# Optimization experiments

Measured on AMD Instinct MI355X. Metric: run time of the kernel, lower is better.

Reference implementation:

```python
import jax, jax.numpy as jnp
import numpy as np

N_HEAD = 16
D_QK = 128
D_V = 128
D_MODEL = 2048
BATCH = 2
SEQ = 2048


def alibi_slopes(n_head):
    # standard ALiBi slopes: 2^(-8*i/n_head) for i = 1..n_head
    return jnp.asarray(2.0 ** (-8.0 * np.arange(1, n_head + 1) / n_head), dtype=jnp.float32)


def setup_inputs() -> dict:
    key = jax.random.key(0)
    k1, k2, k3, k4, k5 = jax.random.split(key, 5)
    x = jax.random.normal(k1, (BATCH, SEQ, D_MODEL), dtype=jnp.float32)
    # causal attention mask (1 = keep, 0 = masked), broadcast over heads
    causal = jnp.tril(jnp.ones((SEQ, SEQ), dtype=bool))
    attention_mask = jnp.broadcast_to(causal, (BATCH, 1, SEQ, SEQ))
    Wq = jax.random.normal(k2, (D_MODEL, N_HEAD * D_QK), dtype=jnp.float32) * (D_MODEL ** -0.5)
    Wk = jax.random.normal(k3, (D_MODEL, N_HEAD * D_QK), dtype=jnp.float32) * (D_MODEL ** -0.5)
    Wv = jax.random.normal(k4, (D_MODEL, N_HEAD * D_V), dtype=jnp.float32) * (D_MODEL ** -0.5)
    Wo = jax.random.normal(k5, (N_HEAD * D_V, D_MODEL), dtype=jnp.float32) * ((N_HEAD * D_V) ** -0.5)
    return {"x": x, "attention_mask": attention_mask, "Wq": Wq, "Wk": Wk, "Wv": Wv, "Wo": Wo}


def reference(x, attention_mask, Wq, Wk, Wv, Wo):
    B, S, _ = x.shape
    scale = D_QK ** -0.5
    q = (x @ Wq).reshape(B, S, N_HEAD, D_QK).transpose(0, 2, 1, 3)  # [B,H,S,dqk]
    k = (x @ Wk).reshape(B, S, N_HEAD, D_QK).transpose(0, 2, 1, 3)
    v = (x @ Wv).reshape(B, S, N_HEAD, D_V).transpose(0, 2, 1, 3)
    scores = jnp.einsum('bhid,bhjd->bhij', q, k) * scale  # [B,H,S,S]
    # ALiBi bias: slope_h * (j - i), negative penalty for distant past keys
    pos = jnp.arange(S, dtype=jnp.float32)
    rel = pos[None, :] - pos[:, None]  # [S,S]
    slopes = alibi_slopes(N_HEAD)
    scores = scores + slopes[None, :, None, None] * rel[None, None, :, :]
    scores = jnp.where(attention_mask, scores, jnp.float32(-jnp.inf))
    attn = jax.nn.softmax(scores, axis=-1)
    out = jnp.einsum('bhij,bhjd->bhid', attn, v)  # [B,H,S,dv]
    out = out.transpose(0, 2, 1, 3).reshape(B, S, N_HEAD * D_V)
    return out @ Wo
```

## Files before the change

### kernel.cpp

```cpp
#include <hip/hip_runtime.h>
#include <cstdint>

typedef unsigned short u16;
typedef __attribute__((ext_vector_type(4))) u16 u16x4;
typedef __attribute__((ext_vector_type(8))) u16 u16x8;
typedef __attribute__((ext_vector_type(8))) __bf16 bf16x8;
typedef __attribute__((ext_vector_type(4))) float f32x4;

#define LOG2E 1.44269504088896340736f

static __device__ __forceinline__ u16 f2bf(float f) {
  unsigned u = __builtin_bit_cast(unsigned, f);
  u += 0x7fffu + ((u >> 16) & 1u);
  return (u16)(u >> 16);
}
static __device__ __forceinline__ float bf2f(u16 v) {
  unsigned u = ((unsigned)v) << 16;
  return __builtin_bit_cast(float, u);
}


static __device__ __forceinline__ void gload16(const u16* g, u16* l) {
  __builtin_amdgcn_global_load_lds(
      (__attribute__((address_space(1))) void*)(uintptr_t)g,
      (__attribute__((address_space(3))) void*)(uintptr_t)l, 16, 0, 0);
}

static __device__ __forceinline__ bf16x8 lds_bf8(const void* p) {
  return __builtin_bit_cast(bf16x8, *(const u16x8*)p);
}

__global__ __launch_bounds__(256) void cast_x_kernel(const float* __restrict__ src,
                                                     u16* __restrict__ dst) {
  int i = (blockIdx.x * 256 + threadIdx.x) * 4;
  float4 v = *(const float4*)(src + i);
  u16x4 r = {f2bf(v.x), f2bf(v.y), f2bf(v.z), f2bf(v.w)};
  *(u16x4*)(dst + i) = r;
}

__global__ __launch_bounds__(256) void transpose_w4_kernel(const float* Wq, const float* Wk,
                                                           const float* Wv, const float* Wo,
                                                           u16* Wqt, u16* Wkt, u16* Wvt,
                                                           u16* Wot) {
  const float* src = blockIdx.z == 0 ? Wq : (blockIdx.z == 1 ? Wk : (blockIdx.z == 2 ? Wv : Wo));
  u16* dst = blockIdx.z == 0 ? Wqt : (blockIdx.z == 1 ? Wkt : (blockIdx.z == 2 ? Wvt : Wot));
  __shared__ float tile[32][33];
  const int n0 = blockIdx.x * 32, k0 = blockIdx.y * 32;
  const int tx = threadIdx.x & 31, ty = threadIdx.x >> 5;
#pragma unroll
  for (int r = 0; r < 4; ++r) {
    int row = r * 8 + ty;
    tile[row][tx] = src[(size_t)(k0 + row) * 2048 + n0 + tx];
  }
  __syncthreads();
#pragma unroll
  for (int r = 0; r < 4; ++r) {
    int row = r * 8 + ty;
    dst[(size_t)(n0 + row) * 2048 + k0 + tx] = f2bf(tile[tx][row]);
  }
}

#define GSTAGE(TILE, KH, BUF)                                                        \
  do {                                                                               \
    const int bk = (TILE) * 64 + (KH) * 32;                                          \
    u16* as_ = &lds[((BUF) * 2 + (KH)) * 8192];                                      \
    u16* bs_ = &lds[32768 + ((BUF) * 2 + (KH)) * 8192];                              \
    gload16(&A[(size_t)(m0 + sr) * 2048 + bk + scu], as_ + tid * 8);                 \
    gload16(&A[(size_t)(m0 + 128 + sr) * 2048 + bk + scu], as_ + 4096 + tid * 8);    \
    gload16(&Bt[(size_t)(n0 + sr) * 2048 + bk + scu], bs_ + tid * 8);                \
    gload16(&Bt[(size_t)(n0 + 128 + sr) * 2048 + bk + scu], bs_ + 4096 + tid * 8);   \
  } while (0)

#define GPH(BUF, KH, STAGE_STMT, VMLIT)                                              \
  do {                                                                               \
    const u16* as_ = &lds[((BUF) * 2 + (KH)) * 8192];                                \
    const u16* bs_ = &lds[32768 + ((BUF) * 2 + (KH)) * 8192];                        \
    bf16x8 af[8], bq[4];                                                             \
    _Pragma("unroll") for (int mf = 0; mf < 8; ++mf) {                               \
      const int ar = wm * 128 + mf * 16 + l16;                                       \
      af[mf] = lds_bf8(&as_[(ar * 32 + lg * 8) ^ xsw]);                              \
    }                                                                                \
    _Pragma("unroll") for (int nf = 0; nf < 4; ++nf) {                               \
      const int br = wn * 64 + nf * 16 + l16;                                        \
      bq[nf] = lds_bf8(&bs_[(br * 32 + lg * 8) ^ xsw]);                              \
    }                                                                                \
    STAGE_STMT;                                                                      \
    asm volatile("s_barrier" ::: "memory");                                          \
    __builtin_amdgcn_s_setprio(1);                                                   \
    _Pragma("unroll") for (int mf = 0; mf < 8; ++mf)                                 \
        _Pragma("unroll") for (int nf = 0; nf < 4; ++nf) acc[mf][nf] =               \
            __builtin_amdgcn_mfma_f32_16x16x32_bf16(af[mf], bq[nf], acc[mf][nf], 0, 0, 0); \
    __builtin_amdgcn_s_setprio(0);                                                   \
    __builtin_amdgcn_sched_barrier(0);                                               \
    asm volatile("s_waitcnt vmcnt(" #VMLIT ")\n\ts_barrier" ::: "memory");           \
  } while (0)

__global__ __launch_bounds__(512, 2) void qkproj_kernel(const u16* __restrict__ xb,
                                                        const u16* __restrict__ Wqt,
                                                        const u16* __restrict__ Wkt,
                                                        u16* __restrict__ Qb,
                                                        u16* __restrict__ Kb) {
  const int n0g = blockIdx.y * 256;
  const u16* Bt = (n0g < 2048) ? Wqt : Wkt;
  u16* Cout = (n0g < 2048) ? Qb : Kb;
  const u16* A = xb;
  const int m0 = blockIdx.x * 256, n0 = n0g & 2047;
  __shared__ u16 lds[65536];
  const int tid = threadIdx.x, lane = tid & 63, w = tid >> 6;
  const int wm = w >> 2, wn = w & 3;
  const int l16 = lane & 15, lg = lane >> 4;
  const int sr = tid >> 2;
  const int scu = (((tid & 3) ^ ((tid >> 2) & 3))) * 8;
  const int xsw = (l16 & 3) * 8;

  f32x4 acc[8][4];
#pragma unroll
  for (int i = 0; i < 8; ++i)
#pragma unroll
    for (int j = 0; j < 4; ++j) acc[i][j] = f32x4{0.f, 0.f, 0.f, 0.f};

  GSTAGE(0, 0, 0);
  GSTAGE(0, 1, 0);
  GSTAGE(1, 0, 1);
  asm volatile("s_waitcnt vmcnt(8)\n\ts_barrier" ::: "memory");
  for (int m2 = 0; m2 < 30; m2 += 2) {
    GPH(0, 0, GSTAGE(m2 + 1, 1, 1), 8);
    GPH(0, 1, GSTAGE(m2 + 2, 0, 0), 8);
    GPH(1, 0, GSTAGE(m2 + 2, 1, 0), 8);
    GPH(1, 1, GSTAGE(m2 + 3, 0, 1), 8);
  }
  GPH(0, 0, GSTAGE(31, 1, 1), 8);
  GPH(0, 1, (void)0, 4);
  GPH(1, 0, (void)0, 0);
  GPH(1, 1, (void)0, 0);

#pragma unroll
  for (int mf = 0; mf < 8; ++mf)
#pragma unroll
    for (int nf = 0; nf < 4; ++nf)
#pragma unroll
      for (int r = 0; r < 4; ++r) {
        const int row = m0 + wm * 128 + mf * 16 + lg * 4 + r;
        const int col = n0 + wn * 64 + nf * 16 + l16;
        size_t off =
            (((size_t)(row >> 11) * 16 + (col >> 7)) * 2048 + (row & 2047)) * 128 + (col & 127);
        Cout[off] = f2bf(acc[mf][nf][r]);
      }
}

#define GSTAGE2(TILE, S)                                                             \
  do {                                                                               \
    const int bk2 = (TILE) * 64;                                                     \
    u16* as_ = &lds[(S) * 16384];                                                    \
    u16* bs_ = &lds[49152 + (S) * 8192];                                             \
    gload16(pA2 + bk2, as_ + tid * 8);                                               \
    gload16(pA2 + bk2 + (size_t)64 * 2048, as_ + 4096 + tid * 8);                    \
    gload16(pA2 + bk2 + (size_t)128 * 2048, as_ + 8192 + tid * 8);                   \
    gload16(pA2 + bk2 + (size_t)192 * 2048, as_ + 12288 + tid * 8);                  \
    gload16(pB2 + bk2, bs_ + tid * 8);                                               \
    gload16(pB2 + bk2 + (size_t)64 * 2048, bs_ + 4096 + tid * 8);                    \
  } while (0)

#define GPH2(S, STAGE_STMT, VMLIT)                                                   \
  do {                                                                               \
    const char* as_ = (const char*)&lds[(S) * 16384];                                \
    const char* bs_ = (const char*)&lds[49152 + (S) * 8192];                         \
    bf16x8 af[2][8], bq[2][2];                                                       \
    _Pragma("unroll") for (int kh = 0; kh < 2; ++kh)                                 \
        _Pragma("unroll") for (int mf = 0; mf < 8; ++mf) {                           \
      const int ar = wm * 128 + mf * 16 + l16;                                       \
      af[kh][mf] = lds_bf8(as_ + ((ar * 128 + (kh * 4 + lg) * 16) ^ ((l16 & 7) << 4))); \
    }                                                                                \
    _Pragma("unroll") for (int kh = 0; kh < 2; ++kh)                                 \
        _Pragma("unroll") for (int nf = 0; nf < 2; ++nf) {                           \
      const int br = wn * 32 + nf * 16 + l16;                                        \
      bq[kh][nf] = lds_bf8(bs_ + ((br * 128 + (kh * 4 + lg) * 16) ^ ((l16 & 7) << 4))); \
    }                                                                                \
    STAGE_STMT;                                                                      \
    asm volatile("s_barrier" ::: "memory");                                          \
    __builtin_amdgcn_s_setprio(1);                                                   \
    _Pragma("unroll") for (int kh = 0; kh < 2; ++kh)                                 \
        _Pragma("unroll") for (int mf = 0; mf < 8; ++mf)                             \
            _Pragma("unroll") for (int nf = 0; nf < 2; ++nf) acc[mf][nf] =           \
                __builtin_amdgcn_mfma_f32_16x16x32_bf16(af[kh][mf], bq[kh][nf],      \
                                                        acc[mf][nf], 0, 0, 0);      \
    __builtin_amdgcn_s_setprio(0);                                                   \
    __builtin_amdgcn_sched_barrier(0);                                               \
    asm volatile("s_waitcnt vmcnt(" #VMLIT ")\n\ts_barrier" ::: "memory");           \
  } while (0)

template <int MODE>
__device__ __forceinline__ void gemm_dp2(const u16* __restrict__ A, const u16* __restrict__ Bt,
                                         void* __restrict__ Cout, int m0, int n0) {
  __shared__ u16 lds[73728];
  const int tid = threadIdx.x, lane = tid & 63, w = tid >> 6;
  const int wm = w >> 2, wn = w & 3;
  const int l16 = lane & 15, lg = lane >> 4;
  const int scol2 = ((tid & 7) ^ ((tid >> 3) & 7)) * 8;
  const u16* pA2 = A + (size_t)(m0 + (tid >> 3)) * 2048 + scol2;
  const u16* pB2 = Bt + (size_t)(n0 + (tid >> 3)) * 2048 + scol2;

  f32x4 acc[8][2];
#pragma unroll
  for (int i = 0; i < 8; ++i)
#pragma unroll
    for (int j = 0; j < 2; ++j) acc[i][j] = f32x4{0.f, 0.f, 0.f, 0.f};

  GSTAGE2(0, 0);
  GSTAGE2(1, 1);
  asm volatile("s_waitcnt vmcnt(6)\n\ts_barrier" ::: "memory");
  for (int t = 0; t < 30; t += 3) {
    GPH2(0, GSTAGE2(t + 2, 2), 6);
    GPH2(1, GSTAGE2(t + 3, 0), 6);
    GPH2(2, GSTAGE2(t + 4, 1), 6);
  }
  GPH2(0, (void)0, 0);
  GPH2(1, (void)0, 0);

#pragma unroll
  for (int mf = 0; mf < 8; ++mf)
#pragma unroll
    for (int nf = 0; nf < 2; ++nf)
#pragma unroll
      for (int r = 0; r < 4; ++r) {
        const int row = m0 + wm * 128 + mf * 16 + lg * 4 + r;
        const int col = n0 + wn * 32 + nf * 16 + l16;
        const float v = acc[mf][nf][r];
        if constexpr (MODE == 2) {
          size_t off =
              (((size_t)(col >> 11) * 16 + (row >> 7)) * 128 + (row & 127)) * 2048 + (col & 2047);
          ((u16*)Cout)[off] = f2bf(v);
        } else {
          ((float*)Cout)[(size_t)row * 2048 + col] = v;
        }
      }
}

__global__ __launch_bounds__(512, 1) void vt_kernel(const u16* Wvt, const u16* xb, u16* Vb) {
  gemm_dp2<2>(Wvt, xb, Vb, blockIdx.x * 256, blockIdx.y * 128);
}

__global__ __launch_bounds__(512, 1) void out_kernel(const u16* OA, const u16* Wot, float* C) {
  gemm_dp2<1>(OA, Wot, C, blockIdx.x * 256, blockIdx.y * 128);
}

__global__ __launch_bounds__(256) void attn_kernel(const u16* __restrict__ Q,
                                                   const u16* __restrict__ Kg,
                                                   const u16* __restrict__ Vg,
                                                   u16* __restrict__ O,
                                                   u16* __restrict__ Opart,
                                                   float* __restrict__ Lp) {
  const int tid = threadIdx.x, lane = tid & 63, w = tid >> 6;
  const int l16 = lane & 15, lg = lane >> 4;

  const int u = blockIdx.x >> 5, bh = blockIdx.x & 31;
  int tile, st0, st1, slot = 0;
  bool multi = false;
  if (u == 0) { tile = 17; st0 = 0; st1 = 18; }
  else if (u == 1) { tile = 16; st0 = 0; st1 = 17; }
  else if (u < 30) {
    multi = true;
    const int c = u - 2, ti = c >> 1, ch = c & 1;
    tile = 31 - ti;
    const int s = tile + 1, half = (s + 1) >> 1;
    st0 = ch ? half : 0;
    st1 = ch ? s : half;
    slot = bh * 28 + c;
  } else { tile = 45 - u; st0 = 0; st1 = tile + 1; }

  const int q0 = tile * 64;
  const int h = bh & 15, b = bh >> 4;
  const float sl2 = exp2f(-0.5f * (float)(h + 1)) * LOG2E;
  const float sc2 = 0.08838834764831845f * LOG2E;

  __shared__ u16 Kl[64 * 128];
  __shared__ u16 Vl[128 * 64];
  __shared__ u16 Pl[64 * 64];

  const size_t qk_base = (size_t)bh * 2048 * 128;
  const size_t v_base = (size_t)bh * 128 * 2048;

  const u16* kgs = Kg + qk_base + (size_t)(tid >> 4) * 128 + (((tid & 15) ^ ((tid >> 4) & 7)) * 8);
  const u16* vgs = Vg + v_base + (size_t)(tid >> 3) * 2048 + (((tid & 7) ^ ((tid >> 3) & 7)) * 8);

#define STAGEKV(STX)                                                        \
  do {                                                                      \
    const int j0s = (STX)*64;                                               \
    _Pragma("unroll") for (int s = 0; s < 4; ++s) {                         \
      gload16(kgs + (size_t)(j0s + s * 16) * 128, Kl + s * 2048 + tid * 8); \
      gload16(vgs + (size_t)s * 32 * 2048 + j0s, Vl + s * 2048 + tid * 8);  \
    }                                                                       \
  } while (0)

  STAGEKV(st0);

  bf16x8 qf[4];
#pragma unroll
  for (int ks = 0; ks < 4; ++ks)
    qf[ks] = lds_bf8(&Q[qk_base + (size_t)(q0 + w * 16 + l16) * 128 + ks * 32 + lg * 8]);

  f32x4 oacc[8];
#pragma unroll
  for (int j = 0; j < 8; ++j) oacc[j] = f32x4{0.f, 0.f, 0.f, 0.f};
  float lsum0 = 0.f, lsum1 = 0.f;

  float ab4[4], rsl[4];
#pragma unroll
  for (int nf = 0; nf < 4; ++nf)
    ab4[nf] = (float)(st0 * 64 + nf * 16 - q0 - w * 16 - l16) * sl2;
#pragma unroll
  for (int r = 0; r < 4; ++r) rsl[r] = (float)(lg * 4 + r) * sl2;
  const float abinc = 64.0f * sl2;
  const int qrow = w * 16 + l16;
  const int dmaskb = lg * 4 - w * 16 - l16;

  __syncthreads();

#define ASTEP(MASKED)                                                                     \
  do {                                                                                    \
    f32x4 sacc[4];                                                                        \
    _Pragma("unroll") for (int j = 0; j < 4; ++j) sacc[j] = f32x4{0.f, 0.f, 0.f, 0.f};    \
    __builtin_amdgcn_s_setprio(1);                                                        \
    _Pragma("unroll") for (int ks = 0; ks < 4; ++ks) {                                    \
      bf16x8 kf[4];                                                                       \
      _Pragma("unroll") for (int nf = 0; nf < 4; ++nf) {                                  \
        int j = nf * 16 + l16;                                                            \
        kf[nf] = lds_bf8((char*)Kl + ((j * 256 + (ks * 32 + lg * 8) * 2) ^ ((j & 7) << 4))); \
      }                                                                                   \
      _Pragma("unroll") for (int nf = 0; nf < 4; ++nf) sacc[nf] =                         \
          __builtin_amdgcn_mfma_f32_16x16x32_bf16(kf[nf], qf[ks], sacc[nf], 0, 0, 0);     \
    }                                                                                     \
    __builtin_amdgcn_s_setprio(0);                                                        \
    _Pragma("unroll") for (int nf = 0; nf < 4; ++nf) {                                    \
      float pvv[4];                                                                       \
      _Pragma("unroll") for (int r = 0; r < 4; ++r) {                                     \
        float s2 = fmaf(sacc[nf][r], sc2, ab4[nf] + rsl[r]);                              \
        float pv = exp2f(s2);                                                             \
        if (MASKED) pv = (nf * 16 + r + dmaskb <= 0) ? pv : 0.f;                          \
        pvv[r] = pv;                                                                      \
      }                                                                                   \
      ab4[nf] += abinc;                                                                   \
      lsum0 += pvv[0] + pvv[1];                                                           \
      lsum1 += pvv[2] + pvv[3];                                                           \
      unsigned w0_, w1_;                                                                  \
      asm("v_cvt_pk_bf16_f32 %0, %1, %2" : "=v"(w0_) : "v"(pvv[0]), "v"(pvv[1]));         \
      asm("v_cvt_pk_bf16_f32 %0, %1, %2" : "=v"(w1_) : "v"(pvv[2]), "v"(pvv[3]));         \
      uint2 pw_{w0_, w1_};                                                                \
      *(uint2*)((char*)Pl + ((qrow * 128 + (nf * 16 + lg * 4) * 2) ^ ((qrow & 7) << 4))) = pw_; \
    }                                                                                     \
    __builtin_amdgcn_s_setprio(1);                                                        \
    _Pragma("unroll") for (int ks = 0; ks < 2; ++ks) {                                    \
      bf16x8 pf =                                                                         \
          lds_bf8((char*)Pl + ((qrow * 128 + (ks * 32 + lg * 8) * 2) ^ ((qrow & 7) << 4))); \
      _Pragma("unroll") for (int nf = 0; nf < 8; ++nf) {                                  \
        int d = nf * 16 + l16;                                                            \
        bf16x8 vf =                                                                       \
            lds_bf8((char*)Vl + ((d * 128 + (ks * 32 + lg * 8) * 2) ^ ((d & 7) << 4)));   \
        oacc[nf] = __builtin_amdgcn_mfma_f32_16x16x32_bf16(pf, vf, oacc[nf], 0, 0, 0);    \
      }                                                                                   \
    }                                                                                     \
    __builtin_amdgcn_s_setprio(0);                                                        \
    if (st + 1 < st1) {                                                                   \
      __syncthreads();                                                                    \
      STAGEKV(st + 1);                                                                    \
      __syncthreads();                                                                    \
    }                                                                                     \
  } while (0)

  int st = st0;
  const int bulk_end = min(st1, tile);
  for (; st < bulk_end; ++st) ASTEP(false);
  for (; st < st1; ++st) ASTEP(true);
#undef STAGEKV
#undef ASTEP

  float lr = lsum0 + lsum1;
  lr += __shfl_xor(lr, 16, 64);
  lr += __shfl_xor(lr, 32, 64);

  if (multi) {
    if (lg == 0) Lp[(size_t)slot * 64 + qrow] = lr;
#pragma unroll
    for (int r = 0; r < 4; ++r) {
      const int row = w * 16 + lg * 4 + r;
#pragma unroll
      for (int nf = 0; nf < 8; ++nf)
        Opart[((size_t)slot * 64 + row) * 128 + nf * 16 + l16] = f2bf(oacc[nf][r]);
    }
  } else {
#pragma unroll
    for (int r = 0; r < 4; ++r) {
      const float inv = 1.0f / __shfl(lr, lg * 4 + r, 64);
      const int srow = q0 + w * 16 + lg * 4 + r;
#pragma unroll
      for (int nf = 0; nf < 8; ++nf)
        O[((size_t)b * 2048 + srow) * 2048 + h * 128 + nf * 16 + l16] = f2bf(oacc[nf][r] * inv);
    }
  }
}

__global__ __launch_bounds__(256) void combine_kernel(const u16* __restrict__ Opart,
                                                      const float* __restrict__ Lp,
                                                      u16* __restrict__ O) {
  const int bx = blockIdx.x;
  const int bh = bx / 14, ti = bx % 14;
  const int tile = 31 - ti;
  const int slot0 = bh * 28 + ti * 2, slot1 = slot0 + 1;
  const int b = bh >> 4, h = bh & 15;
  const int q0 = tile * 64;
  const int tid = threadIdx.x;
  const int colg = (tid & 15) * 8, rowb = tid >> 4;
#pragma unroll
  for (int rr = 0; rr < 4; ++rr) {
    const int row = rowb + rr * 16;
    const float l0 = Lp[(size_t)slot0 * 64 + row];
    const float l1 = Lp[(size_t)slot1 * 64 + row];
    const float inv = 1.0f / (l0 + l1);
    u16x8 p0 = *(const u16x8*)&Opart[((size_t)slot0 * 64 + row) * 128 + colg];
    u16x8 p1 = *(const u16x8*)&Opart[((size_t)slot1 * 64 + row) * 128 + colg];
    u16x8 o;
#pragma unroll
    for (int e = 0; e < 8; ++e) o[e] = f2bf((bf2f(p0[e]) + bf2f(p1[e])) * inv);
    *(u16x8*)&O[((size_t)b * 2048 + q0 + row) * 2048 + h * 128 + colg] = o;
  }
}

extern "C" void kernel_launch(void* const* d_in, const int* in_sizes, int n_in, void* d_out,
                              int out_size, void* d_ws, size_t ws_size, hipStream_t stream) {
  const float* x = (const float*)d_in[0];
  const float* Wq = (const float*)d_in[2];
  const float* Wk = (const float*)d_in[3];
  const float* Wv = (const float*)d_in[4];
  const float* Wo = (const float*)d_in[5];
  char* ws = (char*)d_ws;

  const size_t MB = 1048576;
  u16* xb = (u16*)(ws);
  u16* Qb = (u16*)(ws + 16 * MB);
  u16* Kb = (u16*)(ws + 32 * MB);
  u16* Vb = (u16*)(ws + 48 * MB);
  u16* Wqt = (u16*)(ws + 64 * MB);
  u16* Wkt = (u16*)(ws + 72 * MB);
  u16* Wvt = (u16*)(ws + 80 * MB);
  u16* Wot = (u16*)(ws + 88 * MB);
  u16* OA = xb;
  u16* Opart = (u16*)(ws + 72 * MB);
  float* Lpf = (float*)(ws + 72 * MB + 896ull * 64 * 128 * 2);

  cast_x_kernel<<<8192, 256, 0, stream>>>(x, xb);
  transpose_w4_kernel<<<dim3(64, 64, 4), 256, 0, stream>>>(Wq, Wk, Wv, Wo, Wqt, Wkt, Wvt, Wot);
  qkproj_kernel<<<dim3(16, 16), 512, 0, stream>>>(xb, Wqt, Wkt, Qb, Kb);
  vt_kernel<<<dim3(8, 32), 512, 0, stream>>>(Wvt, xb, Vb);
  attn_kernel<<<dim3(1472), 256, 0, stream>>>(Qb, Kb, Vb, OA, Opart, Lpf);
  combine_kernel<<<dim3(448), 256, 0, stream>>>(Opart, Lpf, OA);
  out_kernel<<<dim3(16, 16), 512, 0, stream>>>(OA, Wot, (float*)d_out);
}
```

Baseline: 241.3 us.

## Restructure QK projection GEMM to full 64-wide K stages with double buffering

```diff
diff --git a/kernel.cpp b/kernel.cpp
--- a/kernel.cpp
+++ b/kernel.cpp
@@ -60,42 +60,57 @@
   }
 }
 
-#define GSTAGE(TILE, KH, BUF)                                                        \
+#define QSTAGE(TILE, S)                                                              \
   do {                                                                               \
-    const int bk = (TILE) * 64 + (KH) * 32;                                          \
-    u16* as_ = &lds[((BUF) * 2 + (KH)) * 8192];                                      \
-    u16* bs_ = &lds[32768 + ((BUF) * 2 + (KH)) * 8192];                              \
-    gload16(&A[(size_t)(m0 + sr) * 2048 + bk + scu], as_ + tid * 8);                 \
-    gload16(&A[(size_t)(m0 + 128 + sr) * 2048 + bk + scu], as_ + 4096 + tid * 8);    \
-    gload16(&Bt[(size_t)(n0 + sr) * 2048 + bk + scu], bs_ + tid * 8);                \
-    gload16(&Bt[(size_t)(n0 + 128 + sr) * 2048 + bk + scu], bs_ + 4096 + tid * 8);   \
-  } while (0)
-
-#define GPH(BUF, KH, STAGE_STMT, VMLIT)                                              \
+    const int bkq = (TILE) * 64;                                                     \
+    u16* as_ = &lds[(S) * 16384];                                                    \
+    u16* bs_ = &lds[32768 + (S) * 16384];                                            \
+    gload16(pAq + bkq, as_ + tid * 8);                                               \
+    gload16(pAq + bkq + (size_t)64 * 2048, as_ + 4096 + tid * 8);                    \
+    gload16(pAq + bkq + (size_t)128 * 2048, as_ + 8192 + tid * 8);                   \
+    gload16(pAq + bkq + (size_t)192 * 2048, as_ + 12288 + tid * 8);                  \
+    gload16(pBq + bkq, bs_ + tid * 8);                                               \
+    gload16(pBq + bkq + (size_t)64 * 2048, bs_ + 4096 + tid * 8);                    \
+    gload16(pBq + bkq + (size_t)128 * 2048, bs_ + 8192 + tid * 8);                   \
+    gload16(pBq + bkq + (size_t)192 * 2048, bs_ + 12288 + tid * 8);                  \
+  } while (0)
+
+#define QPH(S, STAGE_STMT)                                                           \
   do {                                                                               \
-    const u16* as_ = &lds[((BUF) * 2 + (KH)) * 8192];                                \
-    const u16* bs_ = &lds[32768 + ((BUF) * 2 + (KH)) * 8192];                        \
-    bf16x8 af[8], bq[4];                                                             \
+    const char* as_ = (const char*)&lds[(S) * 16384];                                \
+    const char* bs_ = (const char*)&lds[32768 + (S) * 16384];                        \
+    bf16x8 af0[8], bq0[4], af1[8], bq1[4];                                           \
     _Pragma("unroll") for (int mf = 0; mf < 8; ++mf) {                               \
       const int ar = wm * 128 + mf * 16 + l16;                                       \
-      af[mf] = lds_bf8(&as_[(ar * 32 + lg * 8) ^ xsw]);                              \
+      af0[mf] = lds_bf8(as_ + ((ar * 128 + lg * 16) ^ ((l16 & 7) << 4)));            \
     }                                                                                \
     _Pragma("unroll") for (int nf = 0; nf < 4; ++nf) {                               \
       const int br = wn * 64 + nf * 16 + l16;                                        \
-      bq[nf] = lds_bf8(&bs_[(br * 32 + lg * 8) ^ xsw]);                              \
+      bq0[nf] = lds_bf8(bs_ + ((br * 128 + lg * 16) ^ ((l16 & 7) << 4)));            \
     }                                                                                \
     STAGE_STMT;                                                                      \
     asm volatile("s_barrier" ::: "memory");                                          \
     __builtin_amdgcn_s_setprio(1);                                                   \
     _Pragma("unroll") for (int mf = 0; mf < 8; ++mf)                                 \
         _Pragma("unroll") for (int nf = 0; nf < 4; ++nf) acc[mf][nf] =               \
-            __builtin_amdgcn_mfma_f32_16x16x32_bf16(af[mf], bq[nf], acc[mf][nf], 0, 0, 0); \
+            __builtin_amdgcn_mfma_f32_16x16x32_bf16(af0[mf], bq0[nf], acc[mf][nf], 0, 0, 0); \
+    _Pragma("unroll") for (int mf = 0; mf < 8; ++mf) {                               \
+      const int ar = wm * 128 + mf * 16 + l16;                                       \
+      af1[mf] = lds_bf8(as_ + ((ar * 128 + (4 + lg) * 16) ^ ((l16 & 7) << 4)));      \
+    }                                                                                \
+    _Pragma("unroll") for (int nf = 0; nf < 4; ++nf) {                               \
+      const int br = wn * 64 + nf * 16 + l16;                                        \
+      bq1[nf] = lds_bf8(bs_ + ((br * 128 + (4 + lg) * 16) ^ ((l16 & 7) << 4)));      \
+    }                                                                                \
+    _Pragma("unroll") for (int mf = 0; mf < 8; ++mf)                                 \
+        _Pragma("unroll") for (int nf = 0; nf < 4; ++nf) acc[mf][nf] =               \
+            __builtin_amdgcn_mfma_f32_16x16x32_bf16(af1[mf], bq1[nf], acc[mf][nf], 0, 0, 0); \
     __builtin_amdgcn_s_setprio(0);                                                   \
     __builtin_amdgcn_sched_barrier(0);                                               \
-    asm volatile("s_waitcnt vmcnt(" #VMLIT ")\n\ts_barrier" ::: "memory");           \
-  } while (0)
-
-__global__ __launch_bounds__(512, 2) void qkproj_kernel(const u16* __restrict__ xb,
+    asm volatile("s_waitcnt vmcnt(0)\n\ts_barrier" ::: "memory");                    \
+  } while (0)
+
+__global__ __launch_bounds__(512, 1) void qkproj_kernel(const u16* __restrict__ xb,
                                                         const u16* __restrict__ Wqt,
                                                         const u16* __restrict__ Wkt,
                                                         u16* __restrict__ Qb,
@@ -103,15 +118,14 @@
   const int n0g = blockIdx.y * 256;
   const u16* Bt = (n0g < 2048) ? Wqt : Wkt;
   u16* Cout = (n0g < 2048) ? Qb : Kb;
-  const u16* A = xb;
   const int m0 = blockIdx.x * 256, n0 = n0g & 2047;
   __shared__ u16 lds[65536];
   const int tid = threadIdx.x, lane = tid & 63, w = tid >> 6;
   const int wm = w >> 2, wn = w & 3;
   const int l16 = lane & 15, lg = lane >> 4;
-  const int sr = tid >> 2;
-  const int scu = (((tid & 3) ^ ((tid >> 2) & 3))) * 8;
-  const int xsw = (l16 & 3) * 8;
+  const int scol2 = ((tid & 7) ^ ((tid >> 3) & 7)) * 8;
+  const u16* pAq = xb + (size_t)(m0 + (tid >> 3)) * 2048 + scol2;
+  const u16* pBq = Bt + (size_t)(n0 + (tid >> 3)) * 2048 + scol2;
 
   f32x4 acc[8][4];
 #pragma unroll
@@ -119,20 +133,14 @@
 #pragma unroll
     for (int j = 0; j < 4; ++j) acc[i][j] = f32x4{0.f, 0.f, 0.f, 0.f};
 
-  GSTAGE(0, 0, 0);
-  GSTAGE(0, 1, 0);
-  GSTAGE(1, 0, 1);
-  asm volatile("s_waitcnt vmcnt(8)\n\ts_barrier" ::: "memory");
-  for (int m2 = 0; m2 < 30; m2 += 2) {
-    GPH(0, 0, GSTAGE(m2 + 1, 1, 1), 8);
-    GPH(0, 1, GSTAGE(m2 + 2, 0, 0), 8);
-    GPH(1, 0, GSTAGE(m2 + 2, 1, 0), 8);
-    GPH(1, 1, GSTAGE(m2 + 3, 0, 1), 8);
-  }
-  GPH(0, 0, GSTAGE(31, 1, 1), 8);
-  GPH(0, 1, (void)0, 4);
-  GPH(1, 0, (void)0, 0);
-  GPH(1, 1, (void)0, 0);
+  QSTAGE(0, 0);
+  asm volatile("s_waitcnt vmcnt(0)\n\ts_barrier" ::: "memory");
+  for (int t = 0; t < 30; t += 2) {
+    QPH(0, QSTAGE(t + 1, 1));
+    QPH(1, QSTAGE(t + 2, 0));
+  }
+  QPH(0, QSTAGE(31, 1));
+  QPH(1, (void)0);
 
 #pragma unroll
   for (int mf = 0; mf < 8; ++mf)
```

Result: no change. 237.1 us, median of 2 (-1.7%).
